# Optimization experiments

Hardware: AMD Instinct MI355X
Metric: run time of the kernel (lower is better)

## Reference

```python
import jax, jax.numpy as jnp
import numpy as np

TEMPERATURE = 10.0
EPS = 1e-12  # torch F.normalize eps


def setup_inputs() -> dict:
    key = jax.random.key(0)
    k1, k2 = jax.random.split(key)
    B, D = 8192, 1024
    text_embeddings = jax.random.normal(k1, (B, D), dtype=jnp.float32)
    image_embeddings = jax.random.normal(k2, (B, D), dtype=jnp.float32)
    bias = jnp.zeros((1,), dtype=jnp.float32)
    return {
        "text_embeddings": text_embeddings,
        "image_embeddings": image_embeddings,
        "bias": bias,
    }


def _normalize(x):
    # matches torch F.normalize(p=2, dim=1): x / max(||x||, eps)
    norm = jnp.linalg.norm(x, axis=-1, keepdims=True)
    return x / jnp.maximum(norm, EPS)


def reference(text_embeddings, image_embeddings, bias):
    B = text_embeddings.shape[0]
    img_n = _normalize(image_embeddings)   # [B, D]
    txt_n = _normalize(text_embeddings)    # [B, D]
    # similarity[i, j] = <img_i, txt_j>
    sim = jnp.einsum('id,jd->ij', img_n, txt_n)          # [B, B]
    logits = sim * (-TEMPERATURE) + bias[0]
    labels = 2.0 * jnp.eye(B, dtype=logits.dtype) - 1.0   # +1 diag, -1 off-diag
    # loss_ij = log(1/(1+exp(label*logit))) = -softplus(label*logit)
    total_loss = -jnp.sum(jax.nn.softplus(labels * logits))
    return -(total_loss / B)
```

## Files before the change

### kernel.cpp

```cpp
#include <hip/hip_runtime.h>
#include <stdint.h>
#include <stddef.h>

#define NROWS 8192
#define DIM   1024
#define TEMP  10.0f

#define BM 256
#define BN 128
#define BK 128

typedef __attribute__((ext_vector_type(8))) int i32x8;
typedef __attribute__((ext_vector_type(16))) float floatx16;

__device__ __forceinline__ void load16_lds(const unsigned char* g, unsigned char* l) {
    __builtin_amdgcn_global_load_lds(
        (__attribute__((address_space(1))) void*)(g),
        (__attribute__((address_space(3))) void*)(l),
        16, 0, 0);
}

__device__ __forceinline__ i32x8 ldfrag(const unsigned char* rowbase, int r7, int kb4) {
    const int o0 = (kb4 ^ r7) << 4;
    union { i32x8 v; int4 q[2]; } u;
    u.q[0] = *(const int4*)(rowbase + o0);
    u.q[1] = *(const int4*)(rowbase + (o0 ^ 16));
    return u.v;
}

__global__ __launch_bounds__(256) void normalize_kernel(
    const float* __restrict__ img, const float* __restrict__ txt,
    unsigned char* __restrict__ imgq, unsigned char* __restrict__ txtq,
    float* __restrict__ out)
{
    const int gw = blockIdx.x * 4 + (threadIdx.x >> 6);
    const int lane = threadIdx.x & 63;
    const float* src;
    unsigned char* dst;
    if (gw < NROWS) {
        src = img + (size_t)gw * DIM;
        dst = imgq + (size_t)gw * DIM;
    } else {
        src = txt + (size_t)(gw - NROWS) * DIM;
        dst = txtq + (size_t)(gw - NROWS) * DIM;
    }
    float4 v[4];
    float ss = 0.f;
#pragma unroll
    for (int c = 0; c < 4; c++) {
        v[c] = ((const float4*)src)[lane + 64 * c];
        ss += v[c].x * v[c].x + v[c].y * v[c].y + v[c].z * v[c].z + v[c].w * v[c].w;
    }
#pragma unroll
    for (int off = 32; off; off >>= 1) ss += __shfl_xor(ss, off);
    const float scale = 1.0f / fmaxf(sqrtf(ss), 1e-12f);
#pragma unroll
    for (int c = 0; c < 4; c++) {
        int p = 0;
        p = __builtin_amdgcn_cvt_pk_fp8_f32(v[c].x * scale, v[c].y * scale, p, false);
        p = __builtin_amdgcn_cvt_pk_fp8_f32(v[c].z * scale, v[c].w * scale, p, true);
        ((int*)dst)[lane + 64 * c] = p;
    }
    if (gw == 0 && lane == 0) out[0] = 0.f;
}

__global__ __launch_bounds__(256, 2) void simloss_kernel(
    const unsigned char* __restrict__ An,
    const unsigned char* __restrict__ Bn,
    const float* __restrict__ bias,
    float* __restrict__ out)
{
    __shared__ unsigned char As[BM * BK];
    __shared__ unsigned char Bs[2][BN * BK];
    __shared__ float red[12];

    const int t = threadIdx.x;
    const int lane = t & 63;
    const int wave = t >> 6;

    const int bid = blockIdx.x;
    const int blockN = (bid & 7) + 8 * ((bid >> 3) & 7);
    const int blockM = bid >> 6;

    const int srow = t >> 3;
    const int g = (t & 7) ^ ((t >> 3) & 7);
    const unsigned char* gA = An + (size_t)(blockM * BM + srow) * DIM + g * 16;
    const unsigned char* gB = Bn + (size_t)(blockN * BN + srow) * DIM + g * 16;
    unsigned char* lA = &As[t * 16];

    const int waveM = (wave >> 1) * 128;
    const int waveN = (wave & 1) * 64;
    const int fr = lane & 31;
    const int fh = lane >> 5;

    const unsigned char* arow[4];
    const unsigned char* brow0[2];
    int ar7[4], br7[2];
#pragma unroll
    for (int mi = 0; mi < 4; mi++) {
        const int r = waveM + mi * 32 + fr;
        arow[mi] = &As[r * BK];
        ar7[mi] = r & 7;
    }
#pragma unroll
    for (int ni = 0; ni < 2; ni++) {
        const int r = waveN + ni * 32 + fr;
        brow0[ni] = &Bs[0][r * BK];
        br7[ni] = r & 7;
    }

    floatx16 acc[4][2];
#pragma unroll
    for (int mi = 0; mi < 4; mi++)
#pragma unroll
        for (int ni = 0; ni < 2; ni++)
            acc[mi][ni] = (floatx16)(0.f);

#pragma unroll
    for (int c = 0; c < 4; c++)
        load16_lds(gB + (size_t)c * 32 * DIM, &Bs[0][t * 16 + c * 4096]);

#pragma unroll
    for (int it = 0; it < DIM / BK; it++) {
        const int k0 = it * BK;
        const int cur = it & 1;
        __syncthreads();
#pragma unroll
        for (int c = 0; c < 8; c++)
            load16_lds(gA + (size_t)c * 32 * DIM + k0, lA + c * 4096);
        if (it < DIM / BK - 1) {
#pragma unroll
            for (int c = 0; c < 4; c++)
                load16_lds(gB + (size_t)c * 32 * DIM + k0 + BK,
                           &Bs[cur ^ 1][t * 16 + c * 4096]);
            asm volatile("s_waitcnt vmcnt(4)" ::: "memory");
        } else {
            asm volatile("s_waitcnt vmcnt(0)" ::: "memory");
        }
        __syncthreads();

        asm volatile("s_setprio 1");
        const int boff = cur * (BN * BK);
#pragma unroll
        for (int ks = 0; ks < 2; ks++) {
            const int kb4 = ks * 4 + fh * 2;
            i32x8 b[2];
#pragma unroll
            for (int ni = 0; ni < 2; ni++)
                b[ni] = ldfrag(brow0[ni] + boff, br7[ni], kb4);
#pragma unroll
            for (int mi = 0; mi < 4; mi++) {
                i32x8 a = ldfrag(arow[mi], ar7[mi], kb4);
#pragma unroll
                for (int ni = 0; ni < 2; ni++)
                    acc[mi][ni] = __builtin_amdgcn_mfma_scale_f32_32x32x64_f8f6f4(
                        a, b[ni], acc[mi][ni],
                        0, 0,
                        0, 0x7f7f7f7f,
                        0, 0x7f7f7f7f);
            }
        }
        asm volatile("s_setprio 0");
    }

    const float bv = bias[0];
    const float c1 = -TEMP * 1.4426950408889634f;
    const float c0 = bv * 1.4426950408889634f;
    float accP = 0.f, accQ = 0.f, accD = 0.f;
    const int gi0 = blockM * BM + waveM + 4 * fh;
    const int gj0 = blockN * BN + waveN + fr;
#pragma unroll
    for (int mi = 0; mi < 4; mi++) {
#pragma unroll
        for (int ni = 0; ni < 2; ni++) {
#pragma unroll
            for (int reg = 0; reg < 16; reg++) {
                float s = acc[mi][ni][reg];
                float w = fmaf(s, c1, c0);
                float e2 = __builtin_amdgcn_exp2f(-fabsf(w));
                accP += __builtin_amdgcn_logf(1.0f + e2);
                accP = fmaf(0.5f, fabsf(w), accP);
                accQ += s;
            }
        }
    }
    const bool diagblk = ((blockN >> 1) == blockM);
    if (diagblk) {
#pragma unroll
        for (int mi = 0; mi < 4; mi++)
#pragma unroll
            for (int ni = 0; ni < 2; ni++)
#pragma unroll
                for (int reg = 0; reg < 16; reg++) {
                    int ig = gi0 + mi * 32 + (reg & 3) + 8 * (reg >> 2);
                    int jg = gj0 + ni * 32;
                    if (ig == jg) accD += acc[mi][ni][reg];
                }
    }
#pragma unroll
    for (int off = 32; off; off >>= 1) {
        accP += __shfl_xor(accP, off);
        accQ += __shfl_xor(accQ, off);
        accD += __shfl_xor(accD, off);
    }
    if (lane == 0) {
        red[wave * 3 + 0] = accP;
        red[wave * 3 + 1] = accQ;
        red[wave * 3 + 2] = accD;
    }
    __syncthreads();
    if (t == 0) {
        float P = red[0] + red[3] + red[6] + red[9];
        float Q = red[1] + red[4] + red[7] + red[10];
        float D = red[2] + red[5] + red[8] + red[11];
        float contrib = fmaf(0.6931471805599453f, P, fmaf(5.0f, Q, -16384.0f * bv));
        if (diagblk) contrib += fmaf(-TEMP, D, 128.0f * bv);
        atomicAdd(out, contrib * (1.0f / 8192.0f));
    }
}

extern "C" void kernel_launch(void* const* d_in, const int* in_sizes, int n_in,
                              void* d_out, int out_size, void* d_ws, size_t ws_size,
                              hipStream_t stream) {
    const float* txt = (const float*)d_in[0];
    const float* img = (const float*)d_in[1];
    const float* bias = (const float*)d_in[2];
    float* out = (float*)d_out;

    unsigned char* imgq = (unsigned char*)d_ws;
    unsigned char* txtq = imgq + (size_t)NROWS * DIM;

    normalize_kernel<<<dim3(2 * NROWS / 4), dim3(256), 0, stream>>>(
        img, txt, imgq, txtq, out);

    simloss_kernel<<<dim3((NROWS / BM) * (NROWS / BN)), dim3(256), 0, stream>>>(
        imgq, txtq, bias, out);
}
```

Baseline: 162.6 us.

## Enlarge output tile to 256x256 and double-buffer both A and B in LDS

The block tile N grows from 128 to 256, so each wave computes a 128x128 region with 4x4 MFMA accumulators. The A operand is now double-buffered in LDS as well, so loads for the next K-step of both A and B overlap with compute. The larger tile raises arithmetic intensity and cuts redundant global loads. In exchange it uses twice the accumulator registers and twice the LDS, so occupancy drops to one block per CU and the grid shrinks to 1024 blocks.

```diff
diff --git a/kernel.cpp b/kernel.cpp
--- a/kernel.cpp
+++ b/kernel.cpp
@@ -7,7 +7,7 @@
 #define TEMP  10.0f
 
 #define BM 256
-#define BN 128
+#define BN 256
 #define BK 128
 
 typedef __attribute__((ext_vector_type(8))) int i32x8;
@@ -20,8 +20,7 @@
         16, 0, 0);
 }
 
-__device__ __forceinline__ i32x8 ldfrag(const unsigned char* rowbase, int r7, int kb4) {
-    const int o0 = (kb4 ^ r7) << 4;
+__device__ __forceinline__ i32x8 ldfrag(const unsigned char* rowbase, int o0) {
     union { i32x8 v; int4 q[2]; } u;
     u.q[0] = *(const int4*)(rowbase + o0);
     u.q[1] = *(const int4*)(rowbase + (o0 ^ 16));
@@ -64,13 +63,13 @@
     if (gw == 0 && lane == 0) out[0] = 0.f;
 }
 
-__global__ __launch_bounds__(256, 2) void simloss_kernel(
+__global__ __launch_bounds__(256, 1) void simloss_kernel(
     const unsigned char* __restrict__ An,
     const unsigned char* __restrict__ Bn,
     const float* __restrict__ bias,
     float* __restrict__ out)
 {
-    __shared__ unsigned char As[BM * BK];
+    __shared__ unsigned char As[2][BM * BK];
     __shared__ unsigned char Bs[2][BN * BK];
     __shared__ float red[12];
 
@@ -79,80 +78,67 @@
     const int wave = t >> 6;
 
     const int bid = blockIdx.x;
-    const int blockN = (bid & 7) + 8 * ((bid >> 3) & 7);
-    const int blockM = bid >> 6;
+    const int blockN = (bid & 7) + 8 * ((bid >> 3) & 3);
+    const int blockM = bid >> 5;
 
     const int srow = t >> 3;
     const int g = (t & 7) ^ ((t >> 3) & 7);
     const unsigned char* gA = An + (size_t)(blockM * BM + srow) * DIM + g * 16;
     const unsigned char* gB = Bn + (size_t)(blockN * BN + srow) * DIM + g * 16;
-    unsigned char* lA = &As[t * 16];
 
     const int waveM = (wave >> 1) * 128;
-    const int waveN = (wave & 1) * 64;
+    const int waveN = (wave & 1) * 128;
     const int fr = lane & 31;
     const int fh = lane >> 5;
-
-    const unsigned char* arow[4];
-    const unsigned char* brow0[2];
-    int ar7[4], br7[2];
-#pragma unroll
-    for (int mi = 0; mi < 4; mi++) {
-        const int r = waveM + mi * 32 + fr;
-        arow[mi] = &As[r * BK];
-        ar7[mi] = r & 7;
-    }
-#pragma unroll
-    for (int ni = 0; ni < 2; ni++) {
-        const int r = waveN + ni * 32 + fr;
-        brow0[ni] = &Bs[0][r * BK];
-        br7[ni] = r & 7;
-    }
-
-    floatx16 acc[4][2];
+    const int r7 = fr & 7;
+
+    floatx16 acc[4][4];
 #pragma unroll
     for (int mi = 0; mi < 4; mi++)
 #pragma unroll
-        for (int ni = 0; ni < 2; ni++)
+        for (int ni = 0; ni < 4; ni++)
             acc[mi][ni] = (floatx16)(0.f);
 
 #pragma unroll
-    for (int c = 0; c < 4; c++)
+    for (int c = 0; c < 8; c++)
+        load16_lds(gA + (size_t)c * 32 * DIM, &As[0][t * 16 + c * 4096]);
+#pragma unroll
+    for (int c = 0; c < 8; c++)
         load16_lds(gB + (size_t)c * 32 * DIM, &Bs[0][t * 16 + c * 4096]);
 
 #pragma unroll
     for (int it = 0; it < DIM / BK; it++) {
-        const int k0 = it * BK;
         const int cur = it & 1;
         __syncthreads();
-#pragma unroll
-        for (int c = 0; c < 8; c++)
-            load16_lds(gA + (size_t)c * 32 * DIM + k0, lA + c * 4096);
         if (it < DIM / BK - 1) {
-#pragma unroll
-            for (int c = 0; c < 4; c++)
-                load16_lds(gB + (size_t)c * 32 * DIM + k0 + BK,
+            const int k1 = (it + 1) * BK;
+#pragma unroll
+            for (int c = 0; c < 8; c++)
+                load16_lds(gA + (size_t)c * 32 * DIM + k1,
+                           &As[cur ^ 1][t * 16 + c * 4096]);
+#pragma unroll
+            for (int c = 0; c < 8; c++)
+                load16_lds(gB + (size_t)c * 32 * DIM + k1,
                            &Bs[cur ^ 1][t * 16 + c * 4096]);
-            asm volatile("s_waitcnt vmcnt(4)" ::: "memory");
+            asm volatile("s_waitcnt vmcnt(16)" ::: "memory");
         } else {
             asm volatile("s_waitcnt vmcnt(0)" ::: "memory");
         }
         __syncthreads();
 
         asm volatile("s_setprio 1");
-        const int boff = cur * (BN * BK);
 #pragma unroll
         for (int ks = 0; ks < 2; ks++) {
-            const int kb4 = ks * 4 + fh * 2;
-            i32x8 b[2];
-#pragma unroll
-            for (int ni = 0; ni < 2; ni++)
-                b[ni] = ldfrag(brow0[ni] + boff, br7[ni], kb4);
+            const int o0 = ((ks * 4 + fh * 2) ^ r7) << 4;
+            i32x8 b[4];
+#pragma unroll
+            for (int ni = 0; ni < 4; ni++)
+                b[ni] = ldfrag(&Bs[cur][(waveN + ni * 32 + fr) * BK], o0);
 #pragma unroll
             for (int mi = 0; mi < 4; mi++) {
-                i32x8 a = ldfrag(arow[mi], ar7[mi], kb4);
-#pragma unroll
-                for (int ni = 0; ni < 2; ni++)
+                i32x8 a = ldfrag(&As[cur][(waveM + mi * 32 + fr) * BK], o0);
+#pragma unroll
+                for (int ni = 0; ni < 4; ni++)
                     acc[mi][ni] = __builtin_amdgcn_mfma_scale_f32_32x32x64_f8f6f4(
                         a, b[ni], acc[mi][ni],
                         0, 0,
@@ -172,7 +158,7 @@
 #pragma unroll
     for (int mi = 0; mi < 4; mi++) {
 #pragma unroll
-        for (int ni = 0; ni < 2; ni++) {
+        for (int ni = 0; ni < 4; ni++) {
 #pragma unroll
             for (int reg = 0; reg < 16; reg++) {
                 float s = acc[mi][ni][reg];
@@ -184,12 +170,12 @@
             }
         }
     }
-    const bool diagblk = ((blockN >> 1) == blockM);
+    const bool diagblk = (blockN == blockM);
     if (diagblk) {
 #pragma unroll
         for (int mi = 0; mi < 4; mi++)
 #pragma unroll
-            for (int ni = 0; ni < 2; ni++)
+            for (int ni = 0; ni < 4; ni++)
 #pragma unroll
                 for (int reg = 0; reg < 16; reg++) {
                     int ig = gi0 + mi * 32 + (reg & 3) + 8 * (reg >> 2);
@@ -213,8 +199,8 @@
         float P = red[0] + red[3] + red[6] + red[9];
         float Q = red[1] + red[4] + red[7] + red[10];
         float D = red[2] + red[5] + red[8] + red[11];
-        float contrib = fmaf(0.6931471805599453f, P, fmaf(5.0f, Q, -16384.0f * bv));
-        if (diagblk) contrib += fmaf(-TEMP, D, 128.0f * bv);
+        float contrib = fmaf(0.6931471805599453f, P, fmaf(5.0f, Q, -32768.0f * bv));
+        if (diagblk) contrib += fmaf(-TEMP, D, 256.0f * bv);
         atomicAdd(out, contrib * (1.0f / 8192.0f));
     }
 }
```

Measured after the change: 180.5 us. 11.0% more time.
